# Performance work log

Hardware: AMD Instinct MI355X
Metric: run time of the kernel (lower is better)

## Reference

```python
import jax, jax.numpy as jnp
import numpy as np

B, L, D, H, DFF, WS = 8, 16384, 256, 8, 1024, 32
HD = D // H
NW = L // WS


def setup_inputs() -> dict:
    key = jax.random.key(0)
    ks = jax.random.split(key, 12)
    p = lambda k, sh: jax.random.normal(k, sh, jnp.float32) * 0.02
    return {
        "query_em": jax.random.normal(ks[0], (B, L, D), jnp.float32),
        "key_value_em": jax.random.normal(ks[1], (B, L, D), jnp.float32),
        "Wq": p(ks[2], (D, D)), "bq": jnp.zeros((D,), jnp.float32),
        "Wk": p(ks[3], (D, D)), "bk": jnp.zeros((D,), jnp.float32),
        "Wv": p(ks[4], (D, D)), "bv": jnp.zeros((D,), jnp.float32),
        "Wo": p(ks[5], (D, D)), "bo": jnp.zeros((D,), jnp.float32),
        "g1": jnp.ones((D,), jnp.float32), "be1": jnp.zeros((D,), jnp.float32),
        "W1": p(ks[6], (D, DFF)), "bf1": jnp.zeros((DFF,), jnp.float32),
        "W2": p(ks[7], (DFF, D)), "bf2": jnp.zeros((D,), jnp.float32),
        "g2": jnp.ones((D,), jnp.float32), "be2": jnp.zeros((D,), jnp.float32),
    }


def _layernorm(x, g, b):
    m = jnp.mean(x, axis=-1, keepdims=True)
    v = jnp.var(x, axis=-1, keepdims=True)
    return (x - m) * jax.lax.rsqrt(v + 1e-5) * g + b


def _encoder_layer(q, kv, Wq, bq, Wk, bk, Wv, bv, Wo, bo, g1, be1, W1, bf1, W2, bf2, g2, be2):
    # q, kv: [B, NW, WS, D] -- attention only within each window of WS tokens
    b, nw, ws, d = q.shape
    qh = (q @ Wq + bq).reshape(b, nw, ws, H, HD)
    kh = (kv @ Wk + bk).reshape(b, nw, ws, H, HD)
    vh = (kv @ Wv + bv).reshape(b, nw, ws, H, HD)
    scores = jnp.einsum("bnqhd,bnkhd->bnhqk", qh, kh) / np.sqrt(HD).astype(np.float32)
    attn = jax.nn.softmax(scores, axis=-1)
    o = jnp.einsum("bnhqk,bnkhd->bnqhd", attn, vh).reshape(b, nw, ws, d)
    o = o @ Wo + bo
    x = _layernorm(q + o, g1, be1)  # post-LN residual
    f = jax.nn.relu(x @ W1 + bf1) @ W2 + bf2
    return _layernorm(x + f, g2, be2)


def reference(query_em, key_value_em, Wq, bq, Wk, bk, Wv, bv, Wo, bo,
              g1, be1, W1, bf1, W2, bf2, g2, be2):
    params = (Wq, bq, Wk, bk, Wv, bv, Wo, bo, g1, be1, W1, bf1, W2, bf2, g2, be2)
    q = query_em.reshape(B, NW, WS, D)
    kv = key_value_em.reshape(B, NW, WS, D)
    x = _encoder_layer(q, kv, *params)
    # cyclic shift by half a window-count along the window axis, second pass, shift back
    x = jnp.roll(x, -WS // 2, axis=1)
    x = _encoder_layer(x, x, *params)
    x = jnp.roll(x, WS // 2, axis=1)
    return x.reshape(B, L, D)
```

## Files before the change

kernel.cpp:

```cpp
#include <hip/hip_runtime.h>
#include <cstdint>
#include <cstddef>

typedef unsigned short u16;
typedef __bf16 bf16x8 __attribute__((ext_vector_type(8)));
typedef float f32x4 __attribute__((ext_vector_type(4)));
typedef unsigned short u16x8 __attribute__((ext_vector_type(8)));
typedef unsigned short u16x4 __attribute__((ext_vector_type(4)));

__device__ __forceinline__ u16 f2bf(float f) {
  union { float f; unsigned u; } x; x.f = f;
  unsigned r = x.u + 0x7fffu + ((x.u >> 16) & 1u);
  return (u16)(r >> 16);
}
__device__ __forceinline__ float bf2f(u16 u) {
  union { unsigned u; float f; } x; x.u = ((unsigned)u) << 16;
  return x.f;
}
__device__ __forceinline__ void gload16(const void* g, void* l) {
  __builtin_amdgcn_global_load_lds(
      (const __attribute__((address_space(1))) unsigned int*)g,
      (__attribute__((address_space(3))) unsigned int*)l, 16, 0, 0);
}

template<int MODE, int AF32>
__device__ __forceinline__ void gemm_body(
    const void* __restrict__ Ap_, int lda, const u16* __restrict__ Bt,
    const float* __restrict__ bias, u16* __restrict__ C0, int ldc, int coff,
    u16* __restrict__ C2, int vsplit, int N, int K, int gy, int nwg, int o,
    u16* As, u16* Bs)
{
  const int tid  = threadIdx.x;
  const int lane = tid & 63, w = tid >> 6;
  const int lid = (o & 7) * (nwg >> 3) + (o >> 3);
  const int by = lid % gy, bx = lid / gy;
  const int row0 = bx * 128, col0 = by * 128;
  const int wr = (w >> 1) * 64, wc = (w & 1) * 64;
  const int fr = lane & 15, fg = lane >> 4;
  const int srow  = (w << 5) + (lane >> 2);
  const int sslot = (lane & 3) ^ ((lane >> 2) & 3);
  const u16*   Ab = (const u16*)Ap_;
  const float* Af = (const float*)Ap_;
  const int AB = 128 * 32;

  auto stageB = [&](int buf, int k0) {
    #pragma unroll
    for (int h = 0; h < 2; ++h)
      gload16((const char*)Bt + ((size_t)(col0 + srow + h*16) * K + k0) * 2 + sslot*16,
              &Bs[buf*AB + ((w << 5) + h*16) * 32]);
  };
  auto stageA16 = [&](int buf, int k0) {
    #pragma unroll
    for (int h = 0; h < 2; ++h)
      gload16((const char*)Ab + ((size_t)(row0 + srow + h*16) * lda + k0) * 2 + sslot*16,
              &As[buf*AB + ((w << 5) + h*16) * 32]);
  };
  f32x4 pre[2][2];
  auto loadA32 = [&](int k0) {
    #pragma unroll
    for (int p = 0; p < 2; ++p) {
      const int sidx = tid + p*256, rr = sidx >> 2, sl = sidx & 3;
      const float* src = &Af[(size_t)(row0 + rr) * lda + k0 + sl*8];
      pre[p][0] = *(const f32x4*)src;
      pre[p][1] = *(const f32x4*)(src + 4);
    }
  };
  auto writeA32 = [&](int buf) {
    #pragma unroll
    for (int p = 0; p < 2; ++p) {
      const int sidx = tid + p*256, rr = sidx >> 2, sl = sidx & 3;
      u16x8 ov = { f2bf(pre[p][0][0]), f2bf(pre[p][0][1]),
                   f2bf(pre[p][0][2]), f2bf(pre[p][0][3]),
                   f2bf(pre[p][1][0]), f2bf(pre[p][1][1]),
                   f2bf(pre[p][1][2]), f2bf(pre[p][1][3]) };
      *(u16x8*)&As[buf*AB + rr*32 + ((sl ^ (rr & 3)) << 3)] = ov;
    }
  };

  f32x4 acc[4][4] = {};

  if (AF32) { loadA32(0); stageB(0, 0); writeA32(0); }
  else      { stageA16(0, 0); stageB(0, 0); }
  __syncthreads();
  int cur = 0;
  for (int k0 = 0; k0 < K; k0 += 32) {
    const int has_next = (k0 + 32 < K);
    if (has_next) {
      if (AF32) loadA32(k0 + 32);
      else      stageA16(cur ^ 1, k0 + 32);
      stageB(cur ^ 1, k0 + 32);
    }
    bf16x8 af[4], bf[4];
    #pragma unroll
    for (int i = 0; i < 4; ++i) {
      const int r = wr + i*16 + fr;
      af[i] = *(const bf16x8*)&As[cur*AB + r*32 + ((fg ^ (fr & 3)) << 3)];
    }
    #pragma unroll
    for (int j = 0; j < 4; ++j) {
      const int r = wc + j*16 + fr;
      bf[j] = *(const bf16x8*)&Bs[cur*AB + r*32 + ((fg ^ (fr & 3)) << 3)];
    }
    #pragma unroll
    for (int i = 0; i < 4; ++i)
      #pragma unroll
      for (int j = 0; j < 4; ++j)
        acc[i][j] = __builtin_amdgcn_mfma_f32_16x16x32_bf16(af[i], bf[j], acc[i][j], 0, 0, 0);
    if (AF32 && has_next) writeA32(cur ^ 1);
    __syncthreads();
    cur ^= 1;
  }

  const int vpart = (MODE == 3) || (MODE == 2 && col0 >= vsplit);
  #pragma unroll
  for (int j = 0; j < 4; ++j) {
    const int c  = col0 + wc + j*16 + fr;
    const float bv = bias[c];
    #pragma unroll
    for (int i = 0; i < 4; ++i) {
      if (vpart) {
        const int cv = (MODE == 2) ? c - vsplit : c;
        const int rb = row0 + wr + i*16 + fg*4;
        u16x4 vv;
        #pragma unroll
        for (int t = 0; t < 4; ++t) vv[t] = f2bf(acc[i][j][t] + bv);
        *(u16x4*)&C2[((size_t)(rb >> 5) * 256 + cv) * 32 + (rb & 31)] = vv;
      } else {
        #pragma unroll
        for (int t = 0; t < 4; ++t) {
          const int r = row0 + wr + i*16 + fg*4 + t;
          float v = acc[i][j][t] + bv;
          if (MODE == 1) v = v > 0.f ? v : 0.f;
          C0[(size_t)r * ldc + coff + c] = f2bf(v);
        }
      }
    }
  }
}

template<int MODE, int AF32>
__global__ __launch_bounds__(256) void gemm_bt(
    const void* __restrict__ Ap_, int lda, const u16* __restrict__ Bt,
    const float* __restrict__ bias, u16* __restrict__ C0, int ldc, int coff,
    u16* __restrict__ C2, int vsplit, int N, int K, int gy)
{
  __shared__ u16 As[2 * 128 * 32];
  __shared__ u16 Bs[2 * 128 * 32];
  gemm_body<MODE, AF32>(Ap_, lda, Bt, bias, C0, ldc, coff, C2, vsplit,
                        N, K, gy, gridDim.x, blockIdx.x, As, Bs);
}

__global__ __launch_bounds__(256) void gemm_l1(
    const float* __restrict__ query, const float* __restrict__ keyval,
    const u16* __restrict__ WqkvT, const float* __restrict__ bq,
    const float* __restrict__ bkv, u16* __restrict__ QKc,
    u16* __restrict__ Vtc)
{
  __shared__ u16 As[2 * 128 * 32];
  __shared__ u16 Bs[2 * 128 * 32];
  const int o = blockIdx.x;
  if (o < 2048) {
    gemm_body<2, 1>(query, 256, WqkvT, bq, QKc, 512, 0, Vtc, 1 << 30,
                    256, 256, 2, 2048, o, As, Bs);
  } else {
    gemm_body<2, 1>(keyval, 256, WqkvT + 65536, bkv, QKc, 512, 256, Vtc, 256,
                    512, 256, 4, 4096, o - 2048, As, Bs);
  }
}

template<int RES_F32>
__global__ __launch_bounds__(512) void gemm_oln(
    const u16* __restrict__ Ap, int lda, const u16* __restrict__ Bt,
    const float* __restrict__ bias, const void* __restrict__ Res,
    const float* __restrict__ g, const float* __restrict__ be,
    u16* __restrict__ Y, int K)
{
  __shared__ u16 As[2][128 * 32];
  __shared__ u16 Bs[2][256 * 32];
  __shared__ float2 red[128][4];
  __shared__ float2 stats[128];
  const int tid  = threadIdx.x;
  const int lane = tid & 63, w = tid >> 6;
  const int nwg = gridDim.x, o = blockIdx.x;
  const int lid = (o & 7) * (nwg >> 3) + (o >> 3);
  const int row0 = lid * 128;
  const int wr = (w >> 2) * 64, wc = (w & 3) * 64;
  const int fr = lane & 15, fg = lane >> 4;
  const int sr   = lane >> 2;
  const int sslot = (lane & 3) ^ ((lane >> 2) & 3);

  auto stage = [&](int buf, int k0) {
    gload16((const char*)Ap + ((size_t)(row0 + (w << 4) + sr) * lda + k0) * 2 + sslot*16,
            &As[buf][((w << 4)) * 32]);
    #pragma unroll
    for (int h = 0; h < 2; ++h)
      gload16((const char*)Bt + ((size_t)((w << 5) + h*16 + sr) * K + k0) * 2 + sslot*16,
              &Bs[buf][((w << 5) + h*16) * 32]);
  };

  f32x4 acc[4][4] = {};

  stage(0, 0);
  __syncthreads();
  int cur = 0;
  for (int k0 = 0; k0 < K; k0 += 32) {
    if (k0 + 32 < K) stage(cur ^ 1, k0 + 32);
    bf16x8 af[4], bf[4];
    #pragma unroll
    for (int i = 0; i < 4; ++i) {
      const int r = wr + i*16 + fr;
      af[i] = *(const bf16x8*)&As[cur][r*32 + ((fg ^ (fr & 3)) << 3)];
    }
    #pragma unroll
    for (int j = 0; j < 4; ++j) {
      const int r = wc + j*16 + fr;
      bf[j] = *(const bf16x8*)&Bs[cur][r*32 + ((fg ^ (fr & 3)) << 3)];
    }
    #pragma unroll
    for (int i = 0; i < 4; ++i)
      #pragma unroll
      for (int j = 0; j < 4; ++j)
        acc[i][j] = __builtin_amdgcn_mfma_f32_16x16x32_bf16(af[i], bf[j], acc[i][j], 0, 0, 0);
    __syncthreads();
    cur ^= 1;
  }

  float ps[4][4] = {}, pq[4][4] = {};
  #pragma unroll
  for (int j = 0; j < 4; ++j) {
    const int c = wc + j*16 + fr;
    const float bv = bias[c];
    #pragma unroll
    for (int i = 0; i < 4; ++i) {
      #pragma unroll
      for (int t = 0; t < 4; ++t) {
        const int r = row0 + wr + i*16 + fg*4 + t;
        const float rv = RES_F32 ? ((const float*)Res)[(size_t)r * 256 + c]
                                 : bf2f(((const u16*)Res)[(size_t)r * 256 + c]);
        float v = acc[i][j][t] + bv + rv;
        acc[i][j][t] = v;
        ps[i][t] += v;
        pq[i][t] += v * v;
      }
    }
  }
  #pragma unroll
  for (int d = 1; d < 16; d <<= 1) {
    #pragma unroll
    for (int i = 0; i < 4; ++i)
      #pragma unroll
      for (int t = 0; t < 4; ++t) {
        ps[i][t] += __shfl_xor(ps[i][t], d, 64);
        pq[i][t] += __shfl_xor(pq[i][t], d, 64);
      }
  }
  if (fr == 0) {
    #pragma unroll
    for (int i = 0; i < 4; ++i)
      #pragma unroll
      for (int t = 0; t < 4; ++t)
        red[wr + i*16 + fg*4 + t][w & 3] = make_float2(ps[i][t], pq[i][t]);
  }
  __syncthreads();
  if (tid < 128) {
    float S = 0.f, Q = 0.f;
    #pragma unroll
    for (int ww = 0; ww < 4; ++ww) { float2 p = red[tid][ww]; S += p.x; Q += p.y; }
    const float m = S * (1.f/256.f);
    const float var = Q * (1.f/256.f) - m*m;
    stats[tid] = make_float2(m, rsqrtf(var + 1e-5f));
  }
  __syncthreads();
  #pragma unroll
  for (int i = 0; i < 4; ++i) {
    #pragma unroll
    for (int t = 0; t < 4; ++t) {
      const int rl = wr + i*16 + fg*4 + t;
      const float2 st = stats[rl];
      const size_t r = row0 + rl;
      #pragma unroll
      for (int j = 0; j < 4; ++j) {
        const int c = wc + j*16 + fr;
        Y[r * 256 + c] = f2bf((acc[i][j][t] - st.x) * st.y * g[c] + be[c]);
      }
    }
  }
}

template<int OUT_F32>
__global__ __launch_bounds__(512, 2) void ffn_fused(
    const u16* __restrict__ X, const u16* __restrict__ W1T,
    const float* __restrict__ b1, const u16* __restrict__ W2T,
    const float* __restrict__ b2, const float* __restrict__ g,
    const float* __restrict__ be, void* __restrict__ Y)
{
  __shared__ u16 W1s[4][32 * 256];
  __shared__ u16 W2s[4][256 * 32];
  __shared__ u16 Hs[8][32 * 32];
  __shared__ float b1s[1024];
  const int tid = threadIdx.x, lane = tid & 63, w = tid >> 6;
  const int fr = lane & 15, fg = lane >> 4;
  const int row0 = blockIdx.x * 256 + w * 32;
  u16* Hw = &Hs[w][0];
  const int hxor = (fr >> 1) & 3;

  auto stage = [&](int buf, int hb) {
    #pragma unroll
    for (int h = 0; h < 2; ++h) {
      const int r = w*4 + h*2 + (lane >> 5);
      const int sl = (lane & 31) ^ (r & 7);
      gload16((const char*)W1T + ((size_t)((hb << 5) + r) * 256 + sl*8) * 2,
              &W1s[buf][(w*4 + h*2) * 256]);
    }
    #pragma unroll
    for (int h = 0; h < 2; ++h) {
      const int r = w*32 + h*16 + (lane >> 2);
      const int sl = (lane & 3) ^ ((r >> 1) & 3);
      gload16((const char*)W2T + ((size_t)r * 1024 + (hb << 5) + sl*8) * 2,
              &W2s[buf][(w*32 + h*16) * 32]);
    }
  };

  if (tid < 256) {
    f32x4 bv = *(const f32x4*)&b1[tid * 4];
    *(f32x4*)&b1s[tid * 4] = bv;
  }
  bf16x8 af[2][8];
  #pragma unroll
  for (int g2 = 0; g2 < 2; ++g2)
    #pragma unroll
    for (int kf = 0; kf < 8; ++kf)
      af[g2][kf] = *(const bf16x8*)&X[(size_t)(row0 + g2*16 + fr) * 256 + kf*32 + fg*8];
  asm volatile("s_waitcnt vmcnt(0)" ::: "memory");

  f32x4 acc2[2][16] = {};

  auto compute_slice = [&](int hb, int cur) {
    f32x4 acc1[2][2] = {};
    #pragma unroll
    for (int kf = 0; kf < 8; ++kf) {
      #pragma unroll
      for (int hf = 0; hf < 2; ++hf) {
        const int n = hf*16 + fr;
        bf16x8 w1f = *(const bf16x8*)&W1s[cur][n*256 + ((((kf << 2) | fg) ^ (n & 7)) << 3)];
        acc1[hf][0] = __builtin_amdgcn_mfma_f32_16x16x32_bf16(w1f, af[0][kf], acc1[hf][0], 0, 0, 0);
        acc1[hf][1] = __builtin_amdgcn_mfma_f32_16x16x32_bf16(w1f, af[1][kf], acc1[hf][1], 0, 0, 0);
      }
    }
    #pragma unroll
    for (int g2 = 0; g2 < 2; ++g2) {
      #pragma unroll
      for (int hf = 0; hf < 2; ++hf) {
        const int h0 = hf*16 + fg*4;
        f32x4 b4 = *(const f32x4*)&b1s[(hb << 5) + h0];
        u16x4 hv;
        #pragma unroll
        for (int t = 0; t < 4; ++t) {
          float v = acc1[hf][g2][t] + b4[t];
          hv[t] = f2bf(v > 0.f ? v : 0.f);
        }
        const int tok = g2*16 + fr;
        *(u16x4*)((char*)Hw + tok*64 + ((((hf << 1) | (fg >> 1)) ^ hxor) << 4)
                                     + ((fg & 1) << 3)) = hv;
      }
    }
    asm volatile("s_waitcnt lgkmcnt(0)" ::: "memory");
    __builtin_amdgcn_sched_barrier(0);

    bf16x8 hf2[2];
    #pragma unroll
    for (int g2 = 0; g2 < 2; ++g2) {
      const int tok = g2*16 + fr;
      hf2[g2] = *(const bf16x8*)((char*)Hw + tok*64 + ((fg ^ hxor) << 4));
    }
    #pragma unroll
    for (int nf = 0; nf < 16; ++nf) {
      const int n = nf*16 + fr;
      bf16x8 w2f = *(const bf16x8*)&W2s[cur][n*32 + ((fg ^ ((n >> 1) & 3)) << 3)];
      acc2[0][nf] = __builtin_amdgcn_mfma_f32_16x16x32_bf16(hf2[0], w2f, acc2[0][nf], 0, 0, 0);
      acc2[1][nf] = __builtin_amdgcn_mfma_f32_16x16x32_bf16(hf2[1], w2f, acc2[1][nf], 0, 0, 0);
    }
  };

  stage(0, 0);
  stage(1, 1);
  for (int hb = 0; hb < 30; ++hb) {
    stage((hb + 2) & 3, hb + 2);
    asm volatile("s_waitcnt vmcnt(8)" ::: "memory");
    __builtin_amdgcn_s_barrier();
    __builtin_amdgcn_sched_barrier(0);
    compute_slice(hb, hb & 3);
  }
  asm volatile("s_waitcnt vmcnt(4)" ::: "memory");
  __builtin_amdgcn_s_barrier();
  __builtin_amdgcn_sched_barrier(0);
  compute_slice(30, 30 & 3);
  asm volatile("s_waitcnt vmcnt(0)" ::: "memory");
  __builtin_amdgcn_s_barrier();
  __builtin_amdgcn_sched_barrier(0);
  compute_slice(31, 31 & 3);

  #pragma unroll
  for (int g2 = 0; g2 < 2; ++g2) {
    const int rbase = row0 + g2*16 + fg*4;
    float s1[4] = {}, sq[4] = {};
    #pragma unroll
    for (int nf = 0; nf < 16; ++nf) {
      const int c = nf*16 + fr;
      const float b = b2[c];
      #pragma unroll
      for (int t = 0; t < 4; ++t) {
        float v = acc2[g2][nf][t] + b + bf2f(X[(size_t)(rbase + t) * 256 + c]);
        acc2[g2][nf][t] = v;
        s1[t] += v; sq[t] += v * v;
      }
    }
    #pragma unroll
    for (int d = 1; d < 16; d <<= 1) {
      #pragma unroll
      for (int t = 0; t < 4; ++t) {
        s1[t] += __shfl_xor(s1[t], d, 64);
        sq[t] += __shfl_xor(sq[t], d, 64);
      }
    }
    float mean[4], rstd[4];
    #pragma unroll
    for (int t = 0; t < 4; ++t) {
      mean[t] = s1[t] * (1.f/256.f);
      const float var = sq[t] * (1.f/256.f) - mean[t]*mean[t];
      rstd[t] = rsqrtf(var + 1e-5f);
    }
    #pragma unroll
    for (int nf = 0; nf < 16; ++nf) {
      const int c = nf*16 + fr;
      const float gc = g[c], bc = be[c];
      #pragma unroll
      for (int t = 0; t < 4; ++t) {
        const float y = (acc2[g2][nf][t] - mean[t]) * rstd[t] * gc + bc;
        if (OUT_F32) ((float*)Y)[(size_t)(rbase + t) * 256 + c] = y;
        else         ((u16*)Y)[(size_t)(rbase + t) * 256 + c] = f2bf(y);
      }
    }
  }
}

__global__ __launch_bounds__(256) void attn_mfma(
    const u16* Q, int sq, const u16* __restrict__ K, int sk,
    const u16* __restrict__ Vt, u16* O, int so)
{
  __shared__ u16 P[4][32 * 40];
  const int tid = threadIdx.x, lane = tid & 63, w = tid >> 6;
  const int win = blockIdx.x * 4 + w;
  const size_t q0 = (size_t)win * 32;
  const int fr = lane & 15, fg = lane >> 4;
  u16* Pw = &P[w][0];
  const float scale = 0.17677669529663687f;

  for (int h = 0; h < 8; ++h) {
    const int co = h * 32;
    bf16x8 qa[2], kb[2];
    #pragma unroll
    for (int i = 0; i < 2; ++i)
      qa[i] = *(const bf16x8*)&Q[(q0 + i*16 + fr) * sq + co + fg*8];
    #pragma unroll
    for (int j = 0; j < 2; ++j)
      kb[j] = *(const bf16x8*)&K[(q0 + j*16 + fr) * sk + co + fg*8];
    f32x4 s[2][2] = {};
    #pragma unroll
    for (int i = 0; i < 2; ++i)
      #pragma unroll
      for (int j = 0; j < 2; ++j)
        s[i][j] = __builtin_amdgcn_mfma_f32_16x16x32_bf16(qa[i], kb[j], s[i][j], 0, 0, 0);

    float inv[2][4];
    #pragma unroll
    for (int i = 0; i < 2; ++i) {
      #pragma unroll
      for (int t = 0; t < 4; ++t) {
        float a0 = s[i][0][t] * scale, a1 = s[i][1][t] * scale;
        float mx = fmaxf(a0, a1);
        #pragma unroll
        for (int d = 1; d < 16; d <<= 1) mx = fmaxf(mx, __shfl_xor(mx, d, 64));
        const float p0 = __expf(a0 - mx), p1 = __expf(a1 - mx);
        float sm = p0 + p1;
        #pragma unroll
        for (int d = 1; d < 16; d <<= 1) sm += __shfl_xor(sm, d, 64);
        inv[i][t] = 1.f / sm;
        const int q = i*16 + fg*4 + t;
        Pw[q*40 + fr]      = f2bf(p0);
        Pw[q*40 + 16 + fr] = f2bf(p1);
      }
    }

    bf16x8 pa[2], vb[2];
    #pragma unroll
    for (int i = 0; i < 2; ++i)
      pa[i] = *(const bf16x8*)&Pw[(i*16 + fr)*40 + fg*8];
    #pragma unroll
    for (int j = 0; j < 2; ++j)
      vb[j] = *(const bf16x8*)&Vt[(size_t)win*8192 + (co + j*16 + fr)*32 + fg*8];
    f32x4 oacc[2][2] = {};
    #pragma unroll
    for (int i = 0; i < 2; ++i)
      #pragma unroll
      for (int j = 0; j < 2; ++j)
        oacc[i][j] = __builtin_amdgcn_mfma_f32_16x16x32_bf16(pa[i], vb[j], oacc[i][j], 0, 0, 0);

    #pragma unroll
    for (int i = 0; i < 2; ++i)
      #pragma unroll
      for (int j = 0; j < 2; ++j)
        #pragma unroll
        for (int t = 0; t < 4; ++t)
          O[(q0 + i*16 + fg*4 + t) * so + co + j*16 + fr] =
              f2bf(oacc[i][j][t] * inv[i][t]);
  }
}

__global__ __launch_bounds__(256) void wprep_all(
    const float* __restrict__ Wq, const float* __restrict__ Wk,
    const float* __restrict__ Wv, const float* __restrict__ Wo,
    const float* __restrict__ W1, const float* __restrict__ W2,
    const float* __restrict__ bq, const float* __restrict__ bk,
    const float* __restrict__ bv,
    u16* __restrict__ WqkvT, u16* __restrict__ WoT,
    u16* __restrict__ W1T, u16* __restrict__ W2T, float* __restrict__ bqkv)
{
  const int b = blockIdx.x, t = threadIdx.x;
  if (b < 1024) {
    const int which = b >> 8, idx = ((b & 255) << 8) + t;
    const float* W = which == 0 ? Wq : which == 1 ? Wk : which == 2 ? Wv : Wo;
    u16* Wt = which == 3 ? WoT : WqkvT + which * 65536;
    const int k = idx >> 8, n = idx & 255;
    Wt[n * 256 + k] = f2bf(W[idx]);
  } else if (b < 2048) {
    const int idx = ((b - 1024) << 8) + t;
    const int k = idx >> 10, n = idx & 1023;
    W1T[n * 256 + k] = f2bf(W1[idx]);
  } else if (b < 3072) {
    const int idx = ((b - 2048) << 8) + t;
    const int k = idx >> 8, n = idx & 255;
    W2T[n * 1024 + k] = f2bf(W2[idx]);
  } else {
    const int i = ((b - 3072) << 8) + t;
    bqkv[i] = i < 256 ? bq[i] : (i < 512 ? bk[i - 256] : bv[i - 512]);
  }
}

extern "C" void kernel_launch(void* const* d_in, const int* in_sizes, int n_in,
                              void* d_out, int out_size, void* d_ws, size_t ws_size,
                              hipStream_t stream)
{
  const float* query  = (const float*)d_in[0];
  const float* keyval = (const float*)d_in[1];
  const float* Wq = (const float*)d_in[2];  const float* bq  = (const float*)d_in[3];
  const float* Wk = (const float*)d_in[4];  const float* bk  = (const float*)d_in[5];
  const float* Wv = (const float*)d_in[6];  const float* bv  = (const float*)d_in[7];
  const float* Wo = (const float*)d_in[8];  const float* bo  = (const float*)d_in[9];
  const float* g1 = (const float*)d_in[10]; const float* be1 = (const float*)d_in[11];
  const float* W1 = (const float*)d_in[12]; const float* bf1 = (const float*)d_in[13];
  const float* W2 = (const float*)d_in[14]; const float* bf2 = (const float*)d_in[15];
  const float* g2 = (const float*)d_in[16]; const float* be2 = (const float*)d_in[17];

  const int M = 131072;
  char* ws = (char*)d_ws;
  u16*  xcur = (u16*)ws;
  u16*  x1   = (u16*)(ws + (64ull  << 20));
  u16*  QKc  = (u16*)(ws + (256ull << 20));
  u16*  Vtc  = (u16*)(ws + (384ull << 20));
  u16*  WqkvT = (u16*)(ws + (448ull << 20));
  u16*  WoT   = WqkvT + 196608;
  u16*  W1T   = WoT   + 65536;
  u16*  W2T   = W1T   + 262144;
  float* bqkv = (float*)(W2T + 262144);
  float* bkv  = bqkv + 256;

  wprep_all<<<3075, 256, 0, stream>>>(Wq, Wk, Wv, Wo, W1, W2, bq, bk, bv,
                                      WqkvT, WoT, W1T, W2T, bqkv);


  gemm_l1<<<6144, 256, 0, stream>>>(query, keyval, WqkvT, bq, bkv, QKc, Vtc);
  attn_mfma<<<1024, 256, 0, stream>>>(QKc, 512, QKc + 256, 512, Vtc, QKc, 512);
  gemm_oln<1><<<1024, 512, 0, stream>>>(
      QKc, 512, WoT, bo, query, g1, be1, x1, 256);
  ffn_fused<0><<<512, 512, 0, stream>>>(
      x1, W1T, bf1, W2T, bf2, g2, be2, xcur);

  gemm_bt<2,0><<<6144, 256, 0, stream>>>(
      xcur, 256, WqkvT, bqkv, QKc, 512, 0, Vtc, 512, 768, 256, 6);
  attn_mfma<<<1024, 256, 0, stream>>>(QKc, 512, QKc + 256, 512, Vtc, QKc, 512);
  gemm_oln<0><<<1024, 512, 0, stream>>>(
      QKc, 512, WoT, bo, xcur, g1, be1, x1, 256);
  ffn_fused<1><<<512, 512, 0, stream>>>(
      x1, W1T, bf1, W2T, bf2, g2, be2, d_out);
}
```

Measured before the change: 882.1 us.

## Triple-buffer the fp32-input QKV GEMM with two-deep register prefetch

Splits the fp32-A path of the shared GEMM body into a dedicated pipeline for the first-layer QKV projection. A tiles are prefetched two k-steps ahead into two register sets, B tiles are staged into a three-slot LDS ring, and explicit vmcnt/lgkmcnt waits with a single barrier per step replace the previous double-buffer scheme. The intent is to hide global load latency for the fp32 inputs behind the MFMA work. In exchange it uses more registers and 1.5x the LDS per block, which may lower occupancy, and the hand-written wait counts must match the number of outstanding loads exactly.

```diff
diff --git a/kernel.cpp b/kernel.cpp
--- a/kernel.cpp
+++ b/kernel.cpp
@@ -23,9 +23,93 @@
       (__attribute__((address_space(3))) unsigned int*)l, 16, 0, 0);
 }
 
-template<int MODE, int AF32>
-__device__ __forceinline__ void gemm_body(
-    const void* __restrict__ Ap_, int lda, const u16* __restrict__ Bt,
+template<int MODE>
+__global__ __launch_bounds__(256) void gemm_bt(
+    const u16* __restrict__ Ab, int lda, const u16* __restrict__ Bt,
+    const float* __restrict__ bias, u16* __restrict__ C0, int ldc, int coff,
+    u16* __restrict__ C2, int vsplit, int N, int K, int gy)
+{
+  __shared__ u16 As[2 * 128 * 32];
+  __shared__ u16 Bs[2 * 128 * 32];
+  const int tid  = threadIdx.x;
+  const int lane = tid & 63, w = tid >> 6;
+  const int nwg = gridDim.x, o = blockIdx.x;
+  const int lid = (o & 7) * (nwg >> 3) + (o >> 3);
+  const int by = lid % gy, bx = lid / gy;
+  const int row0 = bx * 128, col0 = by * 128;
+  const int wr = (w >> 1) * 64, wc = (w & 1) * 64;
+  const int fr = lane & 15, fg = lane >> 4;
+  const int srow  = (w << 5) + (lane >> 2);
+  const int sslot = (lane & 3) ^ ((lane >> 2) & 3);
+  const int AB = 128 * 32;
+
+  auto stageB = [&](int buf, int k0) {
+    #pragma unroll
+    for (int h = 0; h < 2; ++h)
+      gload16((const char*)Bt + ((size_t)(col0 + srow + h*16) * K + k0) * 2 + sslot*16,
+              &Bs[buf*AB + ((w << 5) + h*16) * 32]);
+  };
+  auto stageA16 = [&](int buf, int k0) {
+    #pragma unroll
+    for (int h = 0; h < 2; ++h)
+      gload16((const char*)Ab + ((size_t)(row0 + srow + h*16) * lda + k0) * 2 + sslot*16,
+              &As[buf*AB + ((w << 5) + h*16) * 32]);
+  };
+
+  f32x4 acc[4][4] = {};
+
+  stageA16(0, 0); stageB(0, 0);
+  __syncthreads();
+  int cur = 0;
+  for (int k0 = 0; k0 < K; k0 += 32) {
+    if (k0 + 32 < K) { stageA16(cur ^ 1, k0 + 32); stageB(cur ^ 1, k0 + 32); }
+    bf16x8 af[4], bf[4];
+    #pragma unroll
+    for (int i = 0; i < 4; ++i) {
+      const int r = wr + i*16 + fr;
+      af[i] = *(const bf16x8*)&As[cur*AB + r*32 + ((fg ^ (fr & 3)) << 3)];
+    }
+    #pragma unroll
+    for (int j = 0; j < 4; ++j) {
+      const int r = wc + j*16 + fr;
+      bf[j] = *(const bf16x8*)&Bs[cur*AB + r*32 + ((fg ^ (fr & 3)) << 3)];
+    }
+    #pragma unroll
+    for (int i = 0; i < 4; ++i)
+      #pragma unroll
+      for (int j = 0; j < 4; ++j)
+        acc[i][j] = __builtin_amdgcn_mfma_f32_16x16x32_bf16(af[i], bf[j], acc[i][j], 0, 0, 0);
+    __syncthreads();
+    cur ^= 1;
+  }
+
+  const int vpart = (MODE == 2 && col0 >= vsplit);
+  #pragma unroll
+  for (int j = 0; j < 4; ++j) {
+    const int c  = col0 + wc + j*16 + fr;
+    const float bv = bias[c];
+    #pragma unroll
+    for (int i = 0; i < 4; ++i) {
+      if (vpart) {
+        const int cv = c - vsplit;
+        const int rb = row0 + wr + i*16 + fg*4;
+        u16x4 vv;
+        #pragma unroll
+        for (int t = 0; t < 4; ++t) vv[t] = f2bf(acc[i][j][t] + bv);
+        *(u16x4*)&C2[((size_t)(rb >> 5) * 256 + cv) * 32 + (rb & 31)] = vv;
+      } else {
+        #pragma unroll
+        for (int t = 0; t < 4; ++t) {
+          const int r = row0 + wr + i*16 + fg*4 + t;
+          C0[(size_t)r * ldc + coff + c] = f2bf(acc[i][j][t] + bv);
+        }
+      }
+    }
+  }
+}
+
+__device__ __forceinline__ void gemm_f32_pipe(
+    const float* __restrict__ Af, int lda, const u16* __restrict__ Bt,
     const float* __restrict__ bias, u16* __restrict__ C0, int ldc, int coff,
     u16* __restrict__ C2, int vsplit, int N, int K, int gy, int nwg, int o,
     u16* As, u16* Bs)
@@ -39,9 +123,8 @@
   const int fr = lane & 15, fg = lane >> 4;
   const int srow  = (w << 5) + (lane >> 2);
   const int sslot = (lane & 3) ^ ((lane >> 2) & 3);
-  const u16*   Ab = (const u16*)Ap_;
-  const float* Af = (const float*)Ap_;
   const int AB = 128 * 32;
+  const int NT = K >> 5;
 
   auto stageB = [&](int buf, int k0) {
     #pragma unroll
@@ -49,69 +132,72 @@
       gload16((const char*)Bt + ((size_t)(col0 + srow + h*16) * K + k0) * 2 + sslot*16,
               &Bs[buf*AB + ((w << 5) + h*16) * 32]);
   };
-  auto stageA16 = [&](int buf, int k0) {
-    #pragma unroll
-    for (int h = 0; h < 2; ++h)
-      gload16((const char*)Ab + ((size_t)(row0 + srow + h*16) * lda + k0) * 2 + sslot*16,
-              &As[buf*AB + ((w << 5) + h*16) * 32]);
-  };
-  f32x4 pre[2][2];
-  auto loadA32 = [&](int k0) {
+  f32x4 pre[2][2][2];
+  auto loadA32 = [&](int set, int k0) {
     #pragma unroll
     for (int p = 0; p < 2; ++p) {
       const int sidx = tid + p*256, rr = sidx >> 2, sl = sidx & 3;
       const float* src = &Af[(size_t)(row0 + rr) * lda + k0 + sl*8];
-      pre[p][0] = *(const f32x4*)src;
-      pre[p][1] = *(const f32x4*)(src + 4);
-    }
-  };
-  auto writeA32 = [&](int buf) {
+      pre[set][p][0] = *(const f32x4*)src;
+      pre[set][p][1] = *(const f32x4*)(src + 4);
+    }
+  };
+  auto writeA32 = [&](int set, int buf) {
     #pragma unroll
     for (int p = 0; p < 2; ++p) {
       const int sidx = tid + p*256, rr = sidx >> 2, sl = sidx & 3;
-      u16x8 ov = { f2bf(pre[p][0][0]), f2bf(pre[p][0][1]),
-                   f2bf(pre[p][0][2]), f2bf(pre[p][0][3]),
-                   f2bf(pre[p][1][0]), f2bf(pre[p][1][1]),
-                   f2bf(pre[p][1][2]), f2bf(pre[p][1][3]) };
+      u16x8 ov = { f2bf(pre[set][p][0][0]), f2bf(pre[set][p][0][1]),
+                   f2bf(pre[set][p][0][2]), f2bf(pre[set][p][0][3]),
+                   f2bf(pre[set][p][1][0]), f2bf(pre[set][p][1][1]),
+                   f2bf(pre[set][p][1][2]), f2bf(pre[set][p][1][3]) };
       *(u16x8*)&As[buf*AB + rr*32 + ((sl ^ (rr & 3)) << 3)] = ov;
     }
   };
 
   f32x4 acc[4][4] = {};
 
-  if (AF32) { loadA32(0); stageB(0, 0); writeA32(0); }
-  else      { stageA16(0, 0); stageB(0, 0); }
-  __syncthreads();
-  int cur = 0;
-  for (int k0 = 0; k0 < K; k0 += 32) {
-    const int has_next = (k0 + 32 < K);
-    if (has_next) {
-      if (AF32) loadA32(k0 + 32);
-      else      stageA16(cur ^ 1, k0 + 32);
-      stageB(cur ^ 1, k0 + 32);
-    }
+  loadA32(0, 0);
+  loadA32(1, 32);
+  stageB(0, 0);
+  asm volatile("s_waitcnt vmcnt(6)" ::: "memory");
+  writeA32(0, 0);
+  asm volatile("s_waitcnt lgkmcnt(0)" ::: "memory");
+  __builtin_amdgcn_s_barrier();
+  __builtin_amdgcn_sched_barrier(0);
+  stageB(1, 32);
+
+  for (int j = 0; j < NT; ++j) {
+    if (j + 2 < NT) loadA32(j & 1, (j + 2) << 5);
+    if (j + 2 < NT)      asm volatile("s_waitcnt vmcnt(6)" ::: "memory");
+    else if (j + 1 < NT) asm volatile("s_waitcnt vmcnt(2)" ::: "memory");
+    else                 asm volatile("s_waitcnt vmcnt(0)" ::: "memory");
+    if (j + 1 < NT) {
+      writeA32((j + 1) & 1, (j + 1) % 3);
+      asm volatile("s_waitcnt lgkmcnt(0)" ::: "memory");
+    }
+    __builtin_amdgcn_s_barrier();
+    __builtin_amdgcn_sched_barrier(0);
+    if (j + 2 < NT) stageB((j + 2) % 3, (j + 2) << 5);
+    const int cb = j % 3;
     bf16x8 af[4], bf[4];
     #pragma unroll
     for (int i = 0; i < 4; ++i) {
       const int r = wr + i*16 + fr;
-      af[i] = *(const bf16x8*)&As[cur*AB + r*32 + ((fg ^ (fr & 3)) << 3)];
-    }
-    #pragma unroll
-    for (int j = 0; j < 4; ++j) {
-      const int r = wc + j*16 + fr;
-      bf[j] = *(const bf16x8*)&Bs[cur*AB + r*32 + ((fg ^ (fr & 3)) << 3)];
+      af[i] = *(const bf16x8*)&As[cb*AB + r*32 + ((fg ^ (fr & 3)) << 3)];
+    }
+    #pragma unroll
+    for (int j2 = 0; j2 < 4; ++j2) {
+      const int r = wc + j2*16 + fr;
+      bf[j2] = *(const bf16x8*)&Bs[cb*AB + r*32 + ((fg ^ (fr & 3)) << 3)];
     }
     #pragma unroll
     for (int i = 0; i < 4; ++i)
       #pragma unroll
-      for (int j = 0; j < 4; ++j)
-        acc[i][j] = __builtin_amdgcn_mfma_f32_16x16x32_bf16(af[i], bf[j], acc[i][j], 0, 0, 0);
-    if (AF32 && has_next) writeA32(cur ^ 1);
-    __syncthreads();
-    cur ^= 1;
-  }
-
-  const int vpart = (MODE == 3) || (MODE == 2 && col0 >= vsplit);
+      for (int j2 = 0; j2 < 4; ++j2)
+        acc[i][j2] = __builtin_amdgcn_mfma_f32_16x16x32_bf16(af[i], bf[j2], acc[i][j2], 0, 0, 0);
+  }
+
+  const int vpart = (col0 >= vsplit);
   #pragma unroll
   for (int j = 0; j < 4; ++j) {
     const int c  = col0 + wc + j*16 + fr;
@@ -119,7 +205,7 @@
     #pragma unroll
     for (int i = 0; i < 4; ++i) {
       if (vpart) {
-        const int cv = (MODE == 2) ? c - vsplit : c;
+        const int cv = c - vsplit;
         const int rb = row0 + wr + i*16 + fg*4;
         u16x4 vv;
         #pragma unroll
@@ -129,25 +215,11 @@
         #pragma unroll
         for (int t = 0; t < 4; ++t) {
           const int r = row0 + wr + i*16 + fg*4 + t;
-          float v = acc[i][j][t] + bv;
-          if (MODE == 1) v = v > 0.f ? v : 0.f;
-          C0[(size_t)r * ldc + coff + c] = f2bf(v);
+          C0[(size_t)r * ldc + coff + c] = f2bf(acc[i][j][t] + bv);
         }
       }
     }
   }
-}
-
-template<int MODE, int AF32>
-__global__ __launch_bounds__(256) void gemm_bt(
-    const void* __restrict__ Ap_, int lda, const u16* __restrict__ Bt,
-    const float* __restrict__ bias, u16* __restrict__ C0, int ldc, int coff,
-    u16* __restrict__ C2, int vsplit, int N, int K, int gy)
-{
-  __shared__ u16 As[2 * 128 * 32];
-  __shared__ u16 Bs[2 * 128 * 32];
-  gemm_body<MODE, AF32>(Ap_, lda, Bt, bias, C0, ldc, coff, C2, vsplit,
-                        N, K, gy, gridDim.x, blockIdx.x, As, Bs);
 }
 
 __global__ __launch_bounds__(256) void gemm_l1(
@@ -156,15 +228,15 @@
     const float* __restrict__ bkv, u16* __restrict__ QKc,
     u16* __restrict__ Vtc)
 {
-  __shared__ u16 As[2 * 128 * 32];
-  __shared__ u16 Bs[2 * 128 * 32];
+  __shared__ u16 As[3 * 128 * 32];
+  __shared__ u16 Bs[3 * 128 * 32];
   const int o = blockIdx.x;
   if (o < 2048) {
-    gemm_body<2, 1>(query, 256, WqkvT, bq, QKc, 512, 0, Vtc, 1 << 30,
-                    256, 256, 2, 2048, o, As, Bs);
+    gemm_f32_pipe(query, 256, WqkvT, bq, QKc, 512, 0, Vtc, 1 << 30,
+                  256, 256, 2, 2048, o, As, Bs);
   } else {
-    gemm_body<2, 1>(keyval, 256, WqkvT + 65536, bkv, QKc, 512, 256, Vtc, 256,
-                    512, 256, 4, 4096, o - 2048, As, Bs);
+    gemm_f32_pipe(keyval, 256, WqkvT + 65536, bkv, QKc, 512, 256, Vtc, 256,
+                  512, 256, 4, 4096, o - 2048, As, Bs);
   }
 }
 
@@ -586,7 +658,7 @@
   ffn_fused<0><<<512, 512, 0, stream>>>(
       x1, W1T, bf1, W2T, bf2, g2, be2, xcur);
 
-  gemm_bt<2,0><<<6144, 256, 0, stream>>>(
+  gemm_bt<2><<<6144, 256, 0, stream>>>(
       xcur, 256, WqkvT, bqkv, QKc, 512, 0, Vtc, 512, 768, 256, 6);
   attn_mfma<<<1024, 256, 0, stream>>>(QKc, 512, QKc + 256, 512, Vtc, QKc, 512);
   gemm_oln<0><<<1024, 512, 0, stream>>>(
```

New measurement: 881.2 us. Within noise of the previous version (-0.1%).
